# Optimization experiments

Hardware: AMD Instinct MI355X
Metric: run time of the kernel (lower is better)

Reference implementation:

```python
import jax, jax.numpy as jnp
import numpy as np

D_MODEL = 512
N_EXPERTS = 8
TOP_K = 2
B, S = 2, 4096


def setup_inputs() -> dict:
    key = jax.random.key(0)
    ks = jax.random.split(key, 8)
    d, h, e = D_MODEL, 4 * D_MODEL, N_EXPERTS
    sc_in = 1.0 / np.sqrt(d)
    sc_h = 1.0 / np.sqrt(h)
    return {
        "x": jax.random.normal(ks[0], (B, S, d), dtype=jnp.float32),
        "time_stage": jax.random.normal(ks[1], (B, S, d), dtype=jnp.float32),
        "gate_w": jax.random.normal(ks[2], (d, e), dtype=jnp.float32) * sc_in,
        "gate_b": jnp.zeros((e,), dtype=jnp.float32),
        "w1": jax.random.normal(ks[3], (e, d, h), dtype=jnp.float32) * sc_in,
        "b1": jnp.zeros((e, h), dtype=jnp.float32),
        "w2": jax.random.normal(ks[4], (e, h, d), dtype=jnp.float32) * sc_h,
        "b2": jnp.zeros((e, d), dtype=jnp.float32),
    }


def reference(x, time_stage, gate_w, gate_b, w1, b1, w2, b2):
    # Router: softmax over experts of gate(x + stop_grad(TimeStage))
    router_input = x + jax.lax.stop_gradient(time_stage)
    gate_score = jax.nn.softmax(router_input @ gate_w + gate_b, axis=-1)  # [B,S,E]
    topk_val, topk_idx = jax.lax.top_k(gate_score, TOP_K)  # [B,S,K]

    # Per-token per-expert combine weight: sum of top-k probs routed to expert e
    # (zero for non-selected experts) -> [B,S,E]
    onehot = jax.nn.one_hot(topk_idx, N_EXPERTS, dtype=x.dtype)  # [B,S,K,E]
    weights = jnp.einsum("bske,bsk->bse", onehot, topk_val)

    # Dense grouped expert MLP; tokens with zero weight contribute nothing,
    # matching the original masked gather/scatter loop exactly.
    h = jax.nn.gelu(jnp.einsum("bsd,edf->ebsf", x, w1) + b1[:, None, None, :],
                    approximate=False)  # [E,B,S,4D]
    y = jnp.einsum("ebsf,efd->ebsd", h, w2) + b2[:, None, None, :]  # [E,B,S,D]
    out = jnp.einsum("bse,ebsd->bsd", weights, y)
    return out
```

## Files before the change

kernel.cpp:

```cpp
#include <hip/hip_runtime.h>
#include <math.h>

#define D 512
#define H 2048
#define E 8
#define NTOK 8192
#define BK 64
#define PTMAX 17408

typedef __attribute__((ext_vector_type(8))) short bf16x8;
typedef __attribute__((ext_vector_type(4))) float f32x4;

__device__ __forceinline__ short f2b(float v) {
    unsigned u = __float_as_uint(v);
    unsigned r = (u + 0x7FFFu + ((u >> 16) & 1u)) >> 16;
    return (short)r;
}
__device__ __forceinline__ float b2f(short v) {
    unsigned u = ((unsigned)(unsigned short)v) << 16;
    return __uint_as_float(u);
}
__device__ __forceinline__ float gelu_exact(float v) {
    return 0.5f * v * (1.0f + erff(v * 0.70710678118654752f));
}
__device__ __forceinline__ float gelu_fast(float v) {
    float u2 = -1.5957691216f * (v + 0.044715f * v * v * v);
    return v / (1.f + __expf(u2));
}
__device__ __forceinline__ void gll16(const void* g, void* l) {
    __builtin_amdgcn_global_load_lds(
        (const __attribute__((address_space(1))) void*)g,
        (__attribute__((address_space(3))) void*)l, 16, 0, 0);
}
__device__ __forceinline__ void seg_of(const int* cnt, int e, int& s0, int& P) {
    int o = 0;
#pragma unroll
    for (int i = 0; i < E; ++i) {
        int p = (cnt[i] + 127) & ~127;
        if (i < e) o += p;
        if (i == e) P = p;
    }
    s0 = o;
}

__global__ __launch_bounds__(256) void router_score(
    const float* __restrict__ x, const float* __restrict__ ts,
    const float* __restrict__ gw, const float* __restrict__ gb,
    int* __restrict__ sel, float2* __restrict__ wsel,
    short* __restrict__ xbf)
{
    int wave = threadIdx.x >> 6, lane = threadIdx.x & 63;
    int t = blockIdx.x * 4 + wave;

    const float* xr = x + (size_t)t * D + lane * 8;
    const float* tr = ts + (size_t)t * D + lane * 8;
    float4 xa = *reinterpret_cast<const float4*>(xr);
    float4 xb = *reinterpret_cast<const float4*>(xr + 4);
    float4 ta = *reinterpret_cast<const float4*>(tr);
    float4 tb = *reinterpret_cast<const float4*>(tr + 4);

    bf16x8 o;
    o[0] = f2b(xa.x); o[1] = f2b(xa.y); o[2] = f2b(xa.z); o[3] = f2b(xa.w);
    o[4] = f2b(xb.x); o[5] = f2b(xb.y); o[6] = f2b(xb.z); o[7] = f2b(xb.w);
    *reinterpret_cast<bf16x8*>(xbf + (size_t)t * D + lane * 8) = o;

    float v[8] = {xa.x + ta.x, xa.y + ta.y, xa.z + ta.z, xa.w + ta.w,
                  xb.x + tb.x, xb.y + tb.y, xb.z + tb.z, xb.w + tb.w};
    float acc[E];
#pragma unroll
    for (int e2 = 0; e2 < E; ++e2) acc[e2] = 0.f;
#pragma unroll
    for (int i = 0; i < 8; ++i) {
        const float4* gr = reinterpret_cast<const float4*>(gw + (size_t)(lane * 8 + i) * E);
        float4 g0 = gr[0], g1 = gr[1];
        acc[0] += v[i] * g0.x; acc[1] += v[i] * g0.y; acc[2] += v[i] * g0.z; acc[3] += v[i] * g0.w;
        acc[4] += v[i] * g1.x; acc[5] += v[i] * g1.y; acc[6] += v[i] * g1.z; acc[7] += v[i] * g1.w;
    }
#pragma unroll
    for (int m = 32; m; m >>= 1) {
#pragma unroll
        for (int e2 = 0; e2 < E; ++e2) acc[e2] += __shfl_xor(acc[e2], m);
    }
    if (lane == 0) {
        float p[E]; float mx;
#pragma unroll
        for (int e2 = 0; e2 < E; ++e2) p[e2] = acc[e2] + gb[e2];
        mx = p[0];
#pragma unroll
        for (int e2 = 1; e2 < E; ++e2) mx = fmaxf(mx, p[e2]);
        float s = 0.f;
#pragma unroll
        for (int e2 = 0; e2 < E; ++e2) { p[e2] = expf(p[e2] - mx); s += p[e2]; }
        float inv = 1.f / s;
        int i0 = 0; float v0 = p[0];
#pragma unroll
        for (int e2 = 1; e2 < E; ++e2) if (p[e2] > v0) { v0 = p[e2]; i0 = e2; }
        int i1 = (i0 == 0) ? 1 : 0; float v1 = p[i1];
#pragma unroll
        for (int e2 = 0; e2 < E; ++e2)
            if (e2 != i0 && e2 != ((i0 == 0) ? 1 : 0) && p[e2] > v1) { v1 = p[e2]; i1 = e2; }
        sel[t]  = i0 | (i1 << 8);
        wsel[t] = make_float2(v0 * inv, v1 * inv);
    }
}

__global__ __launch_bounds__(256) void scatter_tokens(
    const int* __restrict__ sel, const float2* __restrict__ wsel,
    int* __restrict__ cnt, int* __restrict__ tok_id, float* __restrict__ tok_w)
{
    __shared__ int lh[E];
    __shared__ int gbase[E];
    int tid = threadIdx.x;
    int t = blockIdx.x * 256 + tid;
    if (tid < E) lh[tid] = 0;
    __syncthreads();
    int s = sel[t];
    float2 w = wsel[t];
    int e0 = s & 255, e1 = s >> 8;
    int p0 = atomicAdd(&lh[e0], 1);
    int p1 = atomicAdd(&lh[e1], 1);
    __syncthreads();
    if (tid < E) gbase[tid] = atomicAdd(&cnt[tid], lh[tid]);
    __syncthreads();
    int o0 = gbase[e0] + p0;
    int o1 = gbase[e1] + p1;
    tok_id[e0 * NTOK + o0] = t;
    tok_w [e0 * NTOK + o0] = w.x;
    tok_id[e1 * NTOK + o1] = t;
    tok_w [e1 * NTOK + o1] = w.y;
}

__global__ __launch_bounds__(256) void router_kernel(
    const float* __restrict__ x, const float* __restrict__ ts,
    const float* __restrict__ gw, const float* __restrict__ gb,
    int* __restrict__ cnt, int* __restrict__ tok_id, float* __restrict__ tok_w)
{
    int t = blockIdx.x * blockDim.x + threadIdx.x;
    if (t >= NTOK) return;
    float acc[E];
#pragma unroll
    for (int e = 0; e < E; ++e) acc[e] = gb[e];
    const float* xr = x + (size_t)t * D;
    const float* tr = ts + (size_t)t * D;
#pragma unroll 4
    for (int d = 0; d < D; ++d) {
        float xv = xr[d] + tr[d];
        const float4* g4 = reinterpret_cast<const float4*>(gw + d * E);
        float4 a = g4[0], b = g4[1];
        acc[0] += xv * a.x; acc[1] += xv * a.y; acc[2] += xv * a.z; acc[3] += xv * a.w;
        acc[4] += xv * b.x; acc[5] += xv * b.y; acc[6] += xv * b.z; acc[7] += xv * b.w;
    }
    float m = acc[0];
#pragma unroll
    for (int e = 1; e < E; ++e) m = fmaxf(m, acc[e]);
    float p[E]; float s = 0.f;
#pragma unroll
    for (int e = 0; e < E; ++e) { p[e] = expf(acc[e] - m); s += p[e]; }
    float inv = 1.f / s;
    int i0 = 0; float v0 = p[0];
#pragma unroll
    for (int e = 1; e < E; ++e) if (p[e] > v0) { v0 = p[e]; i0 = e; }
    int i1 = (i0 == 0) ? 1 : 0; float v1 = p[i1];
#pragma unroll
    for (int e = 0; e < E; ++e) if (e != i0 && e != ((i0 == 0) ? 1 : 0) && p[e] > v1) { v1 = p[e]; i1 = e; }
    int pos0 = atomicAdd(&cnt[i0], 1);
    tok_id[i0 * NTOK + pos0] = t;
    tok_w[i0 * NTOK + pos0] = v0 * inv;
    int pos1 = atomicAdd(&cnt[i1], 1);
    tok_id[i1 * NTOK + pos1] = t;
    tok_w[i1 * NTOK + pos1] = v1 * inv;
}

__global__ __launch_bounds__(256) void transpose_pad(
    const float* __restrict__ w1, short* __restrict__ w1t,
    const float* __restrict__ w2, short* __restrict__ w2t,
    const int* __restrict__ cnt, const int* __restrict__ sel,
    const int* __restrict__ tok_id, const float* __restrict__ tok_w,
    int* __restrict__ pad_tok, float* __restrict__ pad_w, int* __restrict__ inv)
{
    int z = blockIdx.z;
    int tid = threadIdx.x;
    if (z == 2 * E) {
        int e = blockIdx.x;
        int i = blockIdx.y * 256 + tid;
        int s, P;
        seg_of(cnt, e, s, P);
        if (i < P) {
            int n = cnt[e];
            int tok = (i < n) ? tok_id[e * NTOK + i] : 0;
            pad_tok[s + i] = tok;
            pad_w[s + i]   = (i < n) ? tok_w[e * NTOK + i] : 0.f;
            if (i < n) {
                int k = ((sel[tok] & 255) == e) ? 0 : 1;
                inv[tok * 2 + k] = s + i;
            }
        }
        return;
    }
    const float* src; short* dst; int R, C, rt, ct;
    if (z < E) {
        src = w1 + (size_t)z * D * H; dst = w1t + (size_t)z * D * H;
        R = D; C = H; rt = blockIdx.x * 64; ct = blockIdx.y * 64;
    } else {
        src = w2 + (size_t)(z - E) * H * D; dst = w2t + (size_t)(z - E) * H * D;
        R = H; C = D; rt = blockIdx.y * 64; ct = blockIdx.x * 64;
    }
    __shared__ float tsb[64][68];
    int r  = tid >> 4;
    int c4 = (tid & 15) * 4;
    for (int rr = r; rr < 64; rr += 16) {
        float4 v = *reinterpret_cast<const float4*>(src + (size_t)(rt + rr) * C + ct + c4);
        tsb[rr][c4] = v.x; tsb[rr][c4 + 1] = v.y; tsb[rr][c4 + 2] = v.z; tsb[rr][c4 + 3] = v.w;
    }
    __syncthreads();
    for (int cr = r; cr < 64; cr += 16) {
        short4 o;
        o.x = f2b(tsb[c4 + 0][cr]);
        o.y = f2b(tsb[c4 + 1][cr]);
        o.z = f2b(tsb[c4 + 2][cr]);
        o.w = f2b(tsb[c4 + 3][cr]);
        *reinterpret_cast<short4*>(dst + (size_t)(ct + cr) * R + rt + c4) = o;
    }
}

__global__ __launch_bounds__(256, 2) void gemm1(
    const short* __restrict__ xbf,
    const short* __restrict__ w1t, const float* __restrict__ b1,
    const int* __restrict__ cnt, const int* __restrict__ pad_tok,
    short* __restrict__ hbuf)
{
    int bid = blockIdx.x;
    int e  = bid & 7;
    int u  = bid >> 3;
    int nt = u & 15;
    int mt = u >> 4;
    int s0, P;
    seg_of(cnt, e, s0, P);
    if (mt * 128 >= P) return;
    int p0 = s0 + mt * 128;

    __shared__ short As[2][128 * BK];
    __shared__ short Bs[2][128 * BK];

    int tid = threadIdx.x;
    int wv = tid >> 6, lane = tid & 63;
    int q = lane >> 4, r = lane & 15;
    int wm = wv >> 1, wn = wv & 1;

    const short* w1e = w1t + (size_t)e * H * D;

    const short* asrc[4];
    const short* bsrc[4];
#pragma unroll
    for (int p = 0; p < 4; ++p) {
        int g = p * 256 + tid;
        int row = g >> 3;
        int slot = (g & 7) ^ (row & 7);
        int tok = pad_tok[p0 + row];
        asrc[p] = xbf + (size_t)tok * D + slot * 8;
        bsrc[p] = w1e + (size_t)(nt * 128 + row) * D + slot * 8;
    }

    f32x4 acc[4][4];
#pragma unroll
    for (int m = 0; m < 4; ++m)
#pragma unroll
        for (int n = 0; n < 4; ++n) acc[m][n] = (f32x4){0.f, 0.f, 0.f, 0.f};

    const int xorv = r & 7;

#pragma unroll
    for (int p = 0; p < 4; ++p) {
        gll16(asrc[p], &As[0][p * 2048 + wv * 512]);
        gll16(bsrc[p], &Bs[0][p * 2048 + wv * 512]);
    }

    const int NTT = D / BK;
    for (int t = 0; t < NTT; ++t) {
        int b = t & 1;
        if (t + 1 < NTT) {
            int kk = (t + 1) * BK;
#pragma unroll
            for (int p = 0; p < 4; ++p) {
                gll16(asrc[p] + kk, &As[b ^ 1][p * 2048 + wv * 512]);
                gll16(bsrc[p] + kk, &Bs[b ^ 1][p * 2048 + wv * 512]);
            }
            asm volatile("s_waitcnt vmcnt(8)" ::: "memory");
        } else {
            asm volatile("s_waitcnt vmcnt(0)" ::: "memory");
        }
        __builtin_amdgcn_s_barrier();
        __builtin_amdgcn_sched_barrier(0);

        const char* Ab = (const char*)&As[b][0];
        const char* Bb = (const char*)&Bs[b][0];
        bf16x8 a[8], bb[8];
#pragma unroll
        for (int ks = 0; ks < 2; ++ks) {
            int sslot = ((ks * 4 + q) ^ xorv) << 4;
#pragma unroll
            for (int m = 0; m < 4; ++m)
                a[ks * 4 + m] = *(const bf16x8*)(Ab + (wm * 64 + m * 16 + r) * 128 + sslot);
#pragma unroll
            for (int n = 0; n < 4; ++n)
                bb[ks * 4 + n] = *(const bf16x8*)(Bb + (wn * 64 + n * 16 + r) * 128 + sslot);
        }
        __builtin_amdgcn_s_setprio(1);
#pragma unroll
        for (int ks = 0; ks < 2; ++ks)
#pragma unroll
            for (int m = 0; m < 4; ++m)
#pragma unroll
                for (int n = 0; n < 4; ++n)
                    acc[m][n] = __builtin_amdgcn_mfma_f32_16x16x32_bf16(
                        a[ks * 4 + m], bb[ks * 4 + n], acc[m][n], 0, 0, 0);
        __builtin_amdgcn_s_setprio(0);
        if (t + 1 < NTT) {
            __builtin_amdgcn_s_barrier();
            __builtin_amdgcn_sched_barrier(0);
        }
    }
    __syncthreads();

    const float* b1e = b1 + (size_t)e * H;
    float bv[4];
#pragma unroll
    for (int n = 0; n < 4; ++n) bv[n] = b1e[nt * 128 + wn * 64 + n * 16 + r];
    short* slab = &As[0][0];
#pragma unroll
    for (int m = 0; m < 4; ++m)
#pragma unroll
        for (int j = 0; j < 4; ++j) {
            int lr = wm * 64 + m * 16 + q * 4 + j;
#pragma unroll
            for (int n = 0; n < 4; ++n) {
                int col = wn * 64 + n * 16 + r;
                slab[lr * 128 + col] = f2b(gelu_fast(acc[m][n][j] + bv[n]));
            }
        }
    __syncthreads();
#pragma unroll
    for (int p = 0; p < 8; ++p) {
        int idx = p * 256 + tid;
        int row = idx >> 4;
        int c16 = idx & 15;
        bf16x8 v = *reinterpret_cast<const bf16x8*>(&slab[row * 128 + c16 * 8]);
        *reinterpret_cast<bf16x8*>(&hbuf[(size_t)(p0 + row) * H + nt * 128 + c16 * 8]) = v;
    }
}

__global__ __launch_bounds__(256, 2) void gemm2(
    const short* __restrict__ hbuf,
    const short* __restrict__ w2t, const float* __restrict__ b2,
    const int* __restrict__ cnt,
    short* __restrict__ ybuf)
{
    int bid = blockIdx.x;
    int e  = bid & 7;
    int u  = bid >> 3;
    int nt = u & 3;
    int mt = u >> 2;
    int s0, P;
    seg_of(cnt, e, s0, P);
    if (mt * 128 >= P) return;
    int p0 = s0 + mt * 128;

    __shared__ short As[2][128 * BK];
    __shared__ short Bs[2][128 * BK];

    int tid = threadIdx.x;
    int wv = tid >> 6, lane = tid & 63;
    int q = lane >> 4, r = lane & 15;
    int wm = wv >> 1, wn = wv & 1;

    const short* w2e = w2t + (size_t)e * D * H;

    const short* asrc[4];
    const short* bsrc[4];
#pragma unroll
    for (int p = 0; p < 4; ++p) {
        int g = p * 256 + tid;
        int row = g >> 3;
        int slot = (g & 7) ^ (row & 7);
        asrc[p] = hbuf + (size_t)(p0 + row) * H + slot * 8;
        bsrc[p] = w2e + (size_t)(nt * 128 + row) * H + slot * 8;
    }

    f32x4 acc[4][4];
#pragma unroll
    for (int m = 0; m < 4; ++m)
#pragma unroll
        for (int n = 0; n < 4; ++n) acc[m][n] = (f32x4){0.f, 0.f, 0.f, 0.f};

    const int xorv = r & 7;

#pragma unroll
    for (int p = 0; p < 4; ++p) {
        gll16(asrc[p], &As[0][p * 2048 + wv * 512]);
        gll16(bsrc[p], &Bs[0][p * 2048 + wv * 512]);
    }

    const int NTT = H / BK;
    for (int t = 0; t < NTT; ++t) {
        int b = t & 1;
        if (t + 1 < NTT) {
            int kk = (t + 1) * BK;
#pragma unroll
            for (int p = 0; p < 4; ++p) {
                gll16(asrc[p] + kk, &As[b ^ 1][p * 2048 + wv * 512]);
                gll16(bsrc[p] + kk, &Bs[b ^ 1][p * 2048 + wv * 512]);
            }
            asm volatile("s_waitcnt vmcnt(8)" ::: "memory");
        } else {
            asm volatile("s_waitcnt vmcnt(0)" ::: "memory");
        }
        __builtin_amdgcn_s_barrier();
        __builtin_amdgcn_sched_barrier(0);

        const char* Ab = (const char*)&As[b][0];
        const char* Bb = (const char*)&Bs[b][0];
        bf16x8 a[8], bb[8];
#pragma unroll
        for (int ks = 0; ks < 2; ++ks) {
            int sslot = ((ks * 4 + q) ^ xorv) << 4;
#pragma unroll
            for (int m = 0; m < 4; ++m)
                a[ks * 4 + m] = *(const bf16x8*)(Ab + (wm * 64 + m * 16 + r) * 128 + sslot);
#pragma unroll
            for (int n = 0; n < 4; ++n)
                bb[ks * 4 + n] = *(const bf16x8*)(Bb + (wn * 64 + n * 16 + r) * 128 + sslot);
        }
        __builtin_amdgcn_s_setprio(1);
#pragma unroll
        for (int ks = 0; ks < 2; ++ks)
#pragma unroll
            for (int m = 0; m < 4; ++m)
#pragma unroll
                for (int n = 0; n < 4; ++n)
                    acc[m][n] = __builtin_amdgcn_mfma_f32_16x16x32_bf16(
                        a[ks * 4 + m], bb[ks * 4 + n], acc[m][n], 0, 0, 0);
        __builtin_amdgcn_s_setprio(0);
        if (t + 1 < NTT) {
            __builtin_amdgcn_s_barrier();
            __builtin_amdgcn_sched_barrier(0);
        }
    }
    __syncthreads();

    const float* b2e = b2 + (size_t)e * D;
    float bv[4];
#pragma unroll
    for (int n = 0; n < 4; ++n) bv[n] = b2e[nt * 128 + wn * 64 + n * 16 + r];
    short* slab = &As[0][0];
#pragma unroll
    for (int m = 0; m < 4; ++m)
#pragma unroll
        for (int j = 0; j < 4; ++j) {
            int lr = wm * 64 + m * 16 + q * 4 + j;
#pragma unroll
            for (int n = 0; n < 4; ++n) {
                int col = wn * 64 + n * 16 + r;
                slab[lr * 128 + col] = f2b(acc[m][n][j] + bv[n]);
            }
        }
    __syncthreads();
#pragma unroll
    for (int p = 0; p < 8; ++p) {
        int idx = p * 256 + tid;
        int row = idx >> 4;
        int c16 = idx & 15;
        bf16x8 v = *reinterpret_cast<const bf16x8*>(&slab[row * 128 + c16 * 8]);
        *reinterpret_cast<bf16x8*>(&ybuf[(size_t)(p0 + row) * D + nt * 128 + c16 * 8]) = v;
    }
}

__global__ __launch_bounds__(256) void combine(
    const short* __restrict__ ybuf, const int* __restrict__ inv,
    const float2* __restrict__ wsel, float* __restrict__ out)
{
    int gid = blockIdx.x * 256 + threadIdx.x;
    int t  = gid >> 7;
    int c4 = (gid & 127) * 4;
    float2 w = wsel[t];
    int i0 = inv[t * 2], i1 = inv[t * 2 + 1];
    short4 y0 = *reinterpret_cast<const short4*>(ybuf + (size_t)i0 * D + c4);
    short4 y1 = *reinterpret_cast<const short4*>(ybuf + (size_t)i1 * D + c4);
    float4 o;
    o.x = w.x * b2f(y0.x) + w.y * b2f(y1.x);
    o.y = w.x * b2f(y0.y) + w.y * b2f(y1.y);
    o.z = w.x * b2f(y0.z) + w.y * b2f(y1.z);
    o.w = w.x * b2f(y0.w) + w.y * b2f(y1.w);
    *reinterpret_cast<float4*>(out + (size_t)t * D + c4) = o;
}

#define TMM 64
#define FCC 64
#define XPAD 520
#define HPD 72

__global__ __launch_bounds__(512, 2) void ffn_mfma(
    const float* __restrict__ x,
    const short* __restrict__ w1t, const float* __restrict__ b1,
    const short* __restrict__ w2t, const float* __restrict__ b2,
    const int* __restrict__ cnt, const int* __restrict__ tok_id,
    const float* __restrict__ tok_w,
    float* __restrict__ out)
{
    int b = blockIdx.x;
    int e = b & 7;
    int tile = b >> 3;
    int n = cnt[e];
    int start = tile * TMM;
    if (start >= n) return;
    int nvalid = min(TMM, n - start);

    __shared__ short xs[TMM * XPAD];
    __shared__ short hs[TMM * HPD];
    __shared__ int   stok[TMM];
    __shared__ float sw[TMM];

    int tid = threadIdx.x;
    if (tid < TMM) {
        int tok = 0; float w = 0.f;
        if (tid < nvalid) {
            tok = tok_id[e * NTOK + start + tid];
            w   = tok_w[e * NTOK + start + tid];
        }
        stok[tid] = tok; sw[tid] = w;
    }
    __syncthreads();

    for (int idx = tid; idx < TMM * (D / 4); idx += 512) {
        int row = idx >> 7;
        int c4  = (idx & 127) << 2;
        float4 v = *reinterpret_cast<const float4*>(x + (size_t)stok[row] * D + c4);
        short4 o; o.x = f2b(v.x); o.y = f2b(v.y); o.z = f2b(v.z); o.w = f2b(v.w);
        *reinterpret_cast<short4*>(&xs[row * XPAD + c4]) = o;
    }
    __syncthreads();

    const int lane = tid & 63, wave = tid >> 6;
    const int wm = wave >> 2, wn = wave & 3;
    const int q = lane >> 4,  r = lane & 15;

    const short* w1e = w1t + (size_t)e * H * D;
    const short* w2e = w2t + (size_t)e * D * H;
    const float* b1e = b1 + (size_t)e * H;
    const float* b2e = b2 + (size_t)e * D;

    f32x4 acc[2][8];
#pragma unroll
    for (int i = 0; i < 2; ++i)
#pragma unroll
        for (int j = 0; j < 8; ++j) acc[i][j] = (f32x4){0.f, 0.f, 0.f, 0.f};

    for (int fc = 0; fc < H; fc += FCC) {
        int f = fc + wn * 16 + r;
        float b1f = b1e[f];
        f32x4 h0 = {b1f, b1f, b1f, b1f};
        f32x4 h1 = h0;
        const short* wrow = w1e + (size_t)f * D;
        const short* a0p = &xs[(wm * 32 + r) * XPAD + q * 8];
        const short* a1p = a0p + 16 * XPAD;
#pragma unroll
        for (int ks = 0; ks < 16; ++ks) {
            bf16x8 bfr = *reinterpret_cast<const bf16x8*>(wrow + ks * 32 + q * 8);
            bf16x8 a0  = *reinterpret_cast<const bf16x8*>(a0p + ks * 32);
            bf16x8 a1  = *reinterpret_cast<const bf16x8*>(a1p + ks * 32);
            h0 = __builtin_amdgcn_mfma_f32_16x16x32_bf16(a0, bfr, h0, 0, 0, 0);
            h1 = __builtin_amdgcn_mfma_f32_16x16x32_bf16(a1, bfr, h1, 0, 0, 0);
        }
        {
            int c = wn * 16 + r;
#pragma unroll
            for (int j = 0; j < 4; ++j) {
                hs[(wm * 32 + q * 4 + j) * HPD + c]      = f2b(gelu_exact(h0[j]));
                hs[(wm * 32 + 16 + q * 4 + j) * HPD + c] = f2b(gelu_exact(h1[j]));
            }
        }
        __syncthreads();
#pragma unroll
        for (int ks = 0; ks < 2; ++ks) {
            bf16x8 a20 = *reinterpret_cast<const bf16x8*>(&hs[(wm * 32 + r) * HPD + ks * 32 + q * 8]);
            bf16x8 a21 = *reinterpret_cast<const bf16x8*>(&hs[(wm * 32 + 16 + r) * HPD + ks * 32 + q * 8]);
#pragma unroll
            for (int nr = 0; nr < 8; ++nr) {
                int dout = wn * 128 + nr * 16 + r;
                bf16x8 bfr = *reinterpret_cast<const bf16x8*>(
                    w2e + (size_t)dout * H + fc + ks * 32 + q * 8);
                acc[0][nr] = __builtin_amdgcn_mfma_f32_16x16x32_bf16(a20, bfr, acc[0][nr], 0, 0, 0);
                acc[1][nr] = __builtin_amdgcn_mfma_f32_16x16x32_bf16(a21, bfr, acc[1][nr], 0, 0, 0);
            }
        }
        __syncthreads();
    }

#pragma unroll
    for (int mrep = 0; mrep < 2; ++mrep) {
#pragma unroll
        for (int j = 0; j < 4; ++j) {
            int rl = wm * 32 + mrep * 16 + q * 4 + j;
            if (rl < nvalid) {
                float w = sw[rl];
                if (w != 0.f) {
                    float* orow = out + (size_t)stok[rl] * D;
#pragma unroll
                    for (int nr = 0; nr < 8; ++nr) {
                        int dout = wn * 128 + nr * 16 + r;
                        f32x4 a = acc[mrep][nr];
                        atomicAdd(&orow[dout], w * (a[j] + b2e[dout]));
                    }
                }
            }
        }
    }
}

extern "C" void kernel_launch(void* const* d_in, const int* in_sizes, int n_in,
                              void* d_out, int out_size, void* d_ws, size_t ws_size,
                              hipStream_t stream) {
    const float* x  = (const float*)d_in[0];
    const float* ts = (const float*)d_in[1];
    const float* gw = (const float*)d_in[2];
    const float* gb = (const float*)d_in[3];
    const float* w1 = (const float*)d_in[4];
    const float* b1 = (const float*)d_in[5];
    const float* w2 = (const float*)d_in[6];
    const float* b2 = (const float*)d_in[7];
    float* out = (float*)d_out;

    int*    cnt     = (int*)d_ws;
    int*    tok_id  = (int*)((char*)d_ws + 1024);
    float*  tok_w   = (float*)((char*)d_ws + 263168);
    int*    pad_tok = (int*)((char*)d_ws + 525312);
    float*  pad_w   = (float*)((char*)d_ws + 594944);
    int*    sel     = (int*)((char*)d_ws + 665600);
    float2* wsel    = (float2*)((char*)d_ws + 700416);
    int*    inv     = (int*)((char*)d_ws + 765952);
    short*  xbf     = (short*)((char*)d_ws + 1048576);
    short*  w1t     = (short*)((char*)d_ws + 9437184);
    short*  w2t     = (short*)((char*)d_ws + 26214400);
    short*  hbuf    = (short*)((char*)d_ws + 42991616);
    short*  ybuf    = (short*)((char*)d_ws + 1048576);
    const size_t ws_need = 114294784;

    hipMemsetAsync(cnt, 0, 64, stream);

    if (ws_size >= ws_need) {
        router_score<<<NTOK / 4, 256, 0, stream>>>(x, ts, gw, gb, sel, wsel, xbf);
        scatter_tokens<<<NTOK / 256, 256, 0, stream>>>(sel, wsel, cnt, tok_id, tok_w);
        transpose_pad<<<dim3(8, 32, 2 * E + 1), 256, 0, stream>>>(
            w1, w1t, w2, w2t, cnt, sel, tok_id, tok_w, pad_tok, pad_w, inv);
        gemm1<<<E * 64 * 16, 256, 0, stream>>>(xbf, w1t, b1, cnt, pad_tok, hbuf);
        gemm2<<<E * 64 * 4, 256, 0, stream>>>(hbuf, w2t, b2, cnt, ybuf);
        combine<<<NTOK * (D / 4) / 256, 256, 0, stream>>>(ybuf, inv, wsel, out);
    } else {
        hipMemsetAsync(out, 0, (size_t)out_size * sizeof(float), stream);
        short* w1t_f = (short*)((char*)d_ws + (1u << 20));
        short* w2t_f = w1t_f + (size_t)E * D * H;
        router_kernel<<<NTOK / 256, 256, 0, stream>>>(x, ts, gw, gb, cnt, tok_id, tok_w);
        transpose_pad<<<dim3(8, 32, 2 * E), 256, 0, stream>>>(
            w1, w1t_f, w2, w2t_f, cnt, nullptr, nullptr, nullptr,
            nullptr, nullptr, nullptr);
        ffn_mfma<<<(NTOK / TMM) * E, 512, 0, stream>>>(
            x, w1t_f, b1, w2t_f, b2, cnt, tok_id, tok_w, out);
    }
}
```

Measured before the change: 188.2 us.

## Replace LDS double-buffered direct loads with register-staged single-buffer prefetch in expert GEMMs

Both expert GEMM kernels drop the double-buffered global_load_lds path. Each thread now prefetches the next K tile into registers, computes from a single shared buffer, then writes the registers to LDS after a barrier. This halves shared memory per block and raises the occupancy hint from 2 to 3 blocks per CU, aiming to hide latency through more resident waves. The cost is extra VGPR pressure, an extra barrier per iteration, and exposed LDS store time inside the loop.

```diff
diff --git a/kernel.cpp b/kernel.cpp
--- a/kernel.cpp
+++ b/kernel.cpp
@@ -26,11 +26,6 @@
 __device__ __forceinline__ float gelu_fast(float v) {
     float u2 = -1.5957691216f * (v + 0.044715f * v * v * v);
     return v / (1.f + __expf(u2));
-}
-__device__ __forceinline__ void gll16(const void* g, void* l) {
-    __builtin_amdgcn_global_load_lds(
-        (const __attribute__((address_space(1))) void*)g,
-        (__attribute__((address_space(3))) void*)l, 16, 0, 0);
 }
 __device__ __forceinline__ void seg_of(const int* cnt, int e, int& s0, int& P) {
     int o = 0;
@@ -223,7 +218,7 @@
     }
 }
 
-__global__ __launch_bounds__(256, 2) void gemm1(
+__global__ __launch_bounds__(256, 3) void gemm1(
     const short* __restrict__ xbf,
     const short* __restrict__ w1t, const float* __restrict__ b1,
     const int* __restrict__ cnt, const int* __restrict__ pad_tok,
@@ -239,11 +234,11 @@
     if (mt * 128 >= P) return;
     int p0 = s0 + mt * 128;
 
-    __shared__ short As[2][128 * BK];
-    __shared__ short Bs[2][128 * BK];
+    __shared__ short lds[16384];
 
     int tid = threadIdx.x;
-    int wv = tid >> 6, lane = tid & 63;
+    int lane = tid & 63;
+    int wv = tid >> 6;
     int q = lane >> 4, r = lane & 15;
     int wm = wv >> 1, wn = wv & 1;
 
@@ -268,56 +263,63 @@
         for (int n = 0; n < 4; ++n) acc[m][n] = (f32x4){0.f, 0.f, 0.f, 0.f};
 
     const int xorv = r & 7;
-
+    const int lw = tid * 8;
+
+    bf16x8 ra[4], rb[4];
 #pragma unroll
     for (int p = 0; p < 4; ++p) {
-        gll16(asrc[p], &As[0][p * 2048 + wv * 512]);
-        gll16(bsrc[p], &Bs[0][p * 2048 + wv * 512]);
-    }
+        ra[p] = *reinterpret_cast<const bf16x8*>(asrc[p]);
+        rb[p] = *reinterpret_cast<const bf16x8*>(bsrc[p]);
+    }
+#pragma unroll
+    for (int p = 0; p < 4; ++p) {
+        *reinterpret_cast<bf16x8*>(&lds[p * 2048 + lw])        = ra[p];
+        *reinterpret_cast<bf16x8*>(&lds[8192 + p * 2048 + lw]) = rb[p];
+    }
+    asm volatile("s_waitcnt lgkmcnt(0)" ::: "memory");
 
     const int NTT = D / BK;
     for (int t = 0; t < NTT; ++t) {
-        int b = t & 1;
         if (t + 1 < NTT) {
             int kk = (t + 1) * BK;
 #pragma unroll
             for (int p = 0; p < 4; ++p) {
-                gll16(asrc[p] + kk, &As[b ^ 1][p * 2048 + wv * 512]);
-                gll16(bsrc[p] + kk, &Bs[b ^ 1][p * 2048 + wv * 512]);
-            }
-            asm volatile("s_waitcnt vmcnt(8)" ::: "memory");
-        } else {
-            asm volatile("s_waitcnt vmcnt(0)" ::: "memory");
+                ra[p] = *reinterpret_cast<const bf16x8*>(asrc[p] + kk);
+                rb[p] = *reinterpret_cast<const bf16x8*>(bsrc[p] + kk);
+            }
         }
         __builtin_amdgcn_s_barrier();
         __builtin_amdgcn_sched_barrier(0);
 
-        const char* Ab = (const char*)&As[b][0];
-        const char* Bb = (const char*)&Bs[b][0];
-        bf16x8 a[8], bb[8];
+        const char* Ab = (const char*)&lds[0];
+        const char* Bb = (const char*)&lds[8192];
 #pragma unroll
         for (int ks = 0; ks < 2; ++ks) {
             int sslot = ((ks * 4 + q) ^ xorv) << 4;
+            bf16x8 a[4], bb[4];
 #pragma unroll
             for (int m = 0; m < 4; ++m)
-                a[ks * 4 + m] = *(const bf16x8*)(Ab + (wm * 64 + m * 16 + r) * 128 + sslot);
+                a[m] = *(const bf16x8*)(Ab + (wm * 64 + m * 16 + r) * 128 + sslot);
 #pragma unroll
             for (int n = 0; n < 4; ++n)
-                bb[ks * 4 + n] = *(const bf16x8*)(Bb + (wn * 64 + n * 16 + r) * 128 + sslot);
-        }
-        __builtin_amdgcn_s_setprio(1);
-#pragma unroll
-        for (int ks = 0; ks < 2; ++ks)
+                bb[n] = *(const bf16x8*)(Bb + (wn * 64 + n * 16 + r) * 128 + sslot);
+            __builtin_amdgcn_s_setprio(1);
 #pragma unroll
             for (int m = 0; m < 4; ++m)
 #pragma unroll
                 for (int n = 0; n < 4; ++n)
-                    acc[m][n] = __builtin_amdgcn_mfma_f32_16x16x32_bf16(
-                        a[ks * 4 + m], bb[ks * 4 + n], acc[m][n], 0, 0, 0);
-        __builtin_amdgcn_s_setprio(0);
+                    acc[m][n] = __builtin_amdgcn_mfma_f32_16x16x32_bf16(a[m], bb[n], acc[m][n], 0, 0, 0);
+            __builtin_amdgcn_s_setprio(0);
+        }
+        __builtin_amdgcn_s_barrier();
+        __builtin_amdgcn_sched_barrier(0);
         if (t + 1 < NTT) {
-            __builtin_amdgcn_s_barrier();
-            __builtin_amdgcn_sched_barrier(0);
+#pragma unroll
+            for (int p = 0; p < 4; ++p) {
+                *reinterpret_cast<bf16x8*>(&lds[p * 2048 + lw])        = ra[p];
+                *reinterpret_cast<bf16x8*>(&lds[8192 + p * 2048 + lw]) = rb[p];
+            }
+            asm volatile("s_waitcnt lgkmcnt(0)" ::: "memory");
         }
     }
     __syncthreads();
@@ -326,7 +328,6 @@
     float bv[4];
 #pragma unroll
     for (int n = 0; n < 4; ++n) bv[n] = b1e[nt * 128 + wn * 64 + n * 16 + r];
-    short* slab = &As[0][0];
 #pragma unroll
     for (int m = 0; m < 4; ++m)
 #pragma unroll
@@ -335,7 +336,7 @@
 #pragma unroll
             for (int n = 0; n < 4; ++n) {
                 int col = wn * 64 + n * 16 + r;
-                slab[lr * 128 + col] = f2b(gelu_fast(acc[m][n][j] + bv[n]));
+                lds[lr * 128 + col] = f2b(gelu_fast(acc[m][n][j] + bv[n]));
             }
         }
     __syncthreads();
@@ -344,12 +345,12 @@
         int idx = p * 256 + tid;
         int row = idx >> 4;
         int c16 = idx & 15;
-        bf16x8 v = *reinterpret_cast<const bf16x8*>(&slab[row * 128 + c16 * 8]);
+        bf16x8 v = *reinterpret_cast<const bf16x8*>(&lds[row * 128 + c16 * 8]);
         *reinterpret_cast<bf16x8*>(&hbuf[(size_t)(p0 + row) * H + nt * 128 + c16 * 8]) = v;
     }
 }
 
-__global__ __launch_bounds__(256, 2) void gemm2(
+__global__ __launch_bounds__(256, 3) void gemm2(
     const short* __restrict__ hbuf,
     const short* __restrict__ w2t, const float* __restrict__ b2,
     const int* __restrict__ cnt,
@@ -365,11 +366,11 @@
     if (mt * 128 >= P) return;
     int p0 = s0 + mt * 128;
 
-    __shared__ short As[2][128 * BK];
-    __shared__ short Bs[2][128 * BK];
+    __shared__ short lds[16384];
 
     int tid = threadIdx.x;
-    int wv = tid >> 6, lane = tid & 63;
+    int lane = tid & 63;
+    int wv = tid >> 6;
     int q = lane >> 4, r = lane & 15;
     int wm = wv >> 1, wn = wv & 1;
 
@@ -393,56 +394,63 @@
         for (int n = 0; n < 4; ++n) acc[m][n] = (f32x4){0.f, 0.f, 0.f, 0.f};
 
     const int xorv = r & 7;
-
+    const int lw = tid * 8;
+
+    bf16x8 ra[4], rb[4];
 #pragma unroll
     for (int p = 0; p < 4; ++p) {
-        gll16(asrc[p], &As[0][p * 2048 + wv * 512]);
-        gll16(bsrc[p], &Bs[0][p * 2048 + wv * 512]);
-    }
+        ra[p] = *reinterpret_cast<const bf16x8*>(asrc[p]);
+        rb[p] = *reinterpret_cast<const bf16x8*>(bsrc[p]);
+    }
+#pragma unroll
+    for (int p = 0; p < 4; ++p) {
+        *reinterpret_cast<bf16x8*>(&lds[p * 2048 + lw])        = ra[p];
+        *reinterpret_cast<bf16x8*>(&lds[8192 + p * 2048 + lw]) = rb[p];
+    }
+    asm volatile("s_waitcnt lgkmcnt(0)" ::: "memory");
 
     const int NTT = H / BK;
     for (int t = 0; t < NTT; ++t) {
-        int b = t & 1;
         if (t + 1 < NTT) {
             int kk = (t + 1) * BK;
 #pragma unroll
             for (int p = 0; p < 4; ++p) {
-                gll16(asrc[p] + kk, &As[b ^ 1][p * 2048 + wv * 512]);
-                gll16(bsrc[p] + kk, &Bs[b ^ 1][p * 2048 + wv * 512]);
-            }
-            asm volatile("s_waitcnt vmcnt(8)" ::: "memory");
-        } else {
-            asm volatile("s_waitcnt vmcnt(0)" ::: "memory");
+                ra[p] = *reinterpret_cast<const bf16x8*>(asrc[p] + kk);
+                rb[p] = *reinterpret_cast<const bf16x8*>(bsrc[p] + kk);
+            }
         }
         __builtin_amdgcn_s_barrier();
         __builtin_amdgcn_sched_barrier(0);
 
-        const char* Ab = (const char*)&As[b][0];
-        const char* Bb = (const char*)&Bs[b][0];
-        bf16x8 a[8], bb[8];
+        const char* Ab = (const char*)&lds[0];
+        const char* Bb = (const char*)&lds[8192];
 #pragma unroll
         for (int ks = 0; ks < 2; ++ks) {
             int sslot = ((ks * 4 + q) ^ xorv) << 4;
+            bf16x8 a[4], bb[4];
 #pragma unroll
             for (int m = 0; m < 4; ++m)
-                a[ks * 4 + m] = *(const bf16x8*)(Ab + (wm * 64 + m * 16 + r) * 128 + sslot);
+                a[m] = *(const bf16x8*)(Ab + (wm * 64 + m * 16 + r) * 128 + sslot);
 #pragma unroll
             for (int n = 0; n < 4; ++n)
-                bb[ks * 4 + n] = *(const bf16x8*)(Bb + (wn * 64 + n * 16 + r) * 128 + sslot);
-        }
-        __builtin_amdgcn_s_setprio(1);
-#pragma unroll
-        for (int ks = 0; ks < 2; ++ks)
+                bb[n] = *(const bf16x8*)(Bb + (wn * 64 + n * 16 + r) * 128 + sslot);
+            __builtin_amdgcn_s_setprio(1);
 #pragma unroll
             for (int m = 0; m < 4; ++m)
 #pragma unroll
                 for (int n = 0; n < 4; ++n)
-                    acc[m][n] = __builtin_amdgcn_mfma_f32_16x16x32_bf16(
-                        a[ks * 4 + m], bb[ks * 4 + n], acc[m][n], 0, 0, 0);
-        __builtin_amdgcn_s_setprio(0);
+                    acc[m][n] = __builtin_amdgcn_mfma_f32_16x16x32_bf16(a[m], bb[n], acc[m][n], 0, 0, 0);
+            __builtin_amdgcn_s_setprio(0);
+        }
+        __builtin_amdgcn_s_barrier();
+        __builtin_amdgcn_sched_barrier(0);
         if (t + 1 < NTT) {
-            __builtin_amdgcn_s_barrier();
-            __builtin_amdgcn_sched_barrier(0);
+#pragma unroll
+            for (int p = 0; p < 4; ++p) {
+                *reinterpret_cast<bf16x8*>(&lds[p * 2048 + lw])        = ra[p];
+                *reinterpret_cast<bf16x8*>(&lds[8192 + p * 2048 + lw]) = rb[p];
+            }
+            asm volatile("s_waitcnt lgkmcnt(0)" ::: "memory");
         }
     }
     __syncthreads();
@@ -451,7 +459,6 @@
     float bv[4];
 #pragma unroll
     for (int n = 0; n < 4; ++n) bv[n] = b2e[nt * 128 + wn * 64 + n * 16 + r];
-    short* slab = &As[0][0];
 #pragma unroll
     for (int m = 0; m < 4; ++m)
 #pragma unroll
@@ -460,7 +467,7 @@
 #pragma unroll
             for (int n = 0; n < 4; ++n) {
                 int col = wn * 64 + n * 16 + r;
-                slab[lr * 128 + col] = f2b(acc[m][n][j] + bv[n]);
+                lds[lr * 128 + col] = f2b(acc[m][n][j] + bv[n]);
             }
         }
     __syncthreads();
@@ -469,7 +476,7 @@
         int idx = p * 256 + tid;
         int row = idx >> 4;
         int c16 = idx & 15;
-        bf16x8 v = *reinterpret_cast<const bf16x8*>(&slab[row * 128 + c16 * 8]);
+        bf16x8 v = *reinterpret_cast<const bf16x8*>(&lds[row * 128 + c16 * 8]);
         *reinterpret_cast<bf16x8*>(&ybuf[(size_t)(p0 + row) * D + nt * 128 + c16 * 8]) = v;
     }
 }
```

Measured after the change: 161.2 us, median of 3. -14.4%, faster.
